# Kernel optimization log

Hardware: AMD Instinct MI355X
Metric: run time of the kernel (lower is better)

Reference implementation:

```python
import jax, jax.numpy as jnp
import numpy as np

EPS = 1e-6
N_HEADS, N_POINTS = 6, 4


def layer_norm(x, w, b):
    m = jnp.mean(x, -1, keepdims=True)
    v = jnp.mean((x - m) ** 2, -1, keepdims=True)
    return (x - m) * jax.lax.rsqrt(v + EPS) * w + b


def bilinear_sample(val, loc, Hl, Wl):
    # val: (B, nH, Hl*Wl, d); loc: (B, Lq, nH, P, 2) in [0,1]
    # matches F.grid_sample(mode='bilinear', padding='zeros', align_corners=False)
    B, nH, _, d = val.shape
    Lq, P = loc.shape[1], loc.shape[3]
    x = loc[..., 0] * Wl - 0.5
    y = loc[..., 1] * Hl - 0.5
    x0 = jnp.floor(x)
    y0 = jnp.floor(y)
    wx1 = x - x0
    wy1 = y - y0
    out = jnp.zeros((B, nH, Lq * P, d), val.dtype)
    corners = ((0, 0, (1 - wy1) * (1 - wx1)), (0, 1, (1 - wy1) * wx1),
               (1, 0, wy1 * (1 - wx1)), (1, 1, wy1 * wx1))
    for dy, dx, w in corners:
        xi = x0 + dx
        yi = y0 + dy
        valid = (xi >= 0) & (xi < Wl) & (yi >= 0) & (yi < Hl)
        xi_c = jnp.clip(xi, 0, Wl - 1).astype(jnp.int32)
        yi_c = jnp.clip(yi, 0, Hl - 1).astype(jnp.int32)
        idx = (yi_c * Wl + xi_c).transpose(0, 2, 1, 3).reshape(B, nH, Lq * P)
        g = jnp.take_along_axis(val, idx[..., None], axis=2)  # (B,nH,Lq*P,d)
        ww = jnp.where(valid, w, 0.0).transpose(0, 2, 1, 3).reshape(B, nH, Lq * P)
        out = out + g * ww[..., None]
    return out.reshape(B, nH, Lq, P, d).transpose(0, 2, 1, 3, 4)  # (B,Lq,nH,P,d)


def dwconv3x3(x, w, b):
    # x: (N, C, H, W); w: (C, 1, 3, 3) depthwise
    y = jax.lax.conv_general_dilated(x, w, (1, 1), 'SAME',
                                     feature_group_count=w.shape[0],
                                     dimension_numbers=('NCHW', 'OIHW', 'NCHW'))
    return y + b[None, :, None, None]


def setup_inputs() -> dict:
    key = jax.random.key(0)
    ks = jax.random.split(key, 16)
    B, H, W, C = 8, 32, 32, 768
    Lq = 3 * H * W
    Hf = Wf = 64
    hidden = int(C * 0.25)
    s = 0.02
    inp = {
        'query': jax.random.normal(ks[0], (B, Lq, C), jnp.float32),
        'reference_points': jax.random.uniform(ks[1], (B, Lq, 1, 2), jnp.float32),
        'feat': jax.random.normal(ks[2], (B, Hf * Wf, C), jnp.float32),
        'spatial_shapes': jnp.array([[Hf, Wf]], jnp.int32),
        'level_start_index': jnp.zeros((1,), jnp.int32),
        'H': H, 'W': W,
        'qn_w': jnp.ones((C,)), 'qn_b': jnp.zeros((C,)),
        'fn_w': jnp.ones((C,)), 'fn_b': jnp.zeros((C,)),
        'so_w': jax.random.normal(ks[3], (C, N_HEADS * N_POINTS * 2)) * s,
        'so_b': jax.random.normal(ks[4], (N_HEADS * N_POINTS * 2,)) * s,
        'aw_w': jax.random.normal(ks[5], (C, N_HEADS * N_POINTS)) * s,
        'aw_b': jnp.zeros((N_HEADS * N_POINTS,)),
        'vp_w': jax.random.normal(ks[6], (C, C)) * s,
        'vp_b': jnp.zeros((C,)),
        'op_w': jax.random.normal(ks[7], (C, C)) * s,
        'op_b': jnp.zeros((C,)),
        'ffn_w': jnp.ones((C,)), 'ffn_b': jnp.zeros((C,)),
        'fc1_w': jax.random.normal(ks[8], (C, hidden)) * s,
        'fc1_b': jnp.zeros((hidden,)),
        'dw_w': jax.random.normal(ks[9], (hidden, 1, 3, 3)) * s,
        'dw_b': jnp.zeros((hidden,)),
        'fc2_w': jax.random.normal(ks[10], (hidden, C)) * s,
        'fc2_b': jnp.zeros((C,)),
    }
    return inp


def reference(query, reference_points, feat, spatial_shapes, level_start_index, H, W,
              qn_w, qn_b, fn_w, fn_b, so_w, so_b, aw_w, aw_b, vp_w, vp_b, op_w, op_b,
              ffn_w, ffn_b, fc1_w, fc1_b, dw_w, dw_b, fc2_w, fc2_b):
    B, Lq, C = query.shape
    nH, nP = N_HEADS, N_POINTS
    d = C // nH
    ss = np.asarray(spatial_shapes)
    Hl, Wl = int(ss[0, 0]), int(ss[0, 1])

    # --- MSDeformAttn (single level) ---
    q = layer_norm(query, qn_w, qn_b)
    f = layer_norm(feat, fn_w, fn_b)
    value = (f @ vp_w + vp_b).reshape(B, Hl * Wl, nH, d).transpose(0, 2, 1, 3)  # (B,nH,Lin,d)
    offs = (q @ so_w + so_b).reshape(B, Lq, nH, 1, nP, 2)
    aw = jax.nn.softmax((q @ aw_w + aw_b).reshape(B, Lq, nH, nP), axis=-1)
    normalizer = jnp.array([Wl, Hl], query.dtype)
    loc = reference_points[:, :, None, :, None, :] + offs / normalizer  # (B,Lq,nH,1,nP,2)
    sampled = bilinear_sample(value, loc[:, :, :, 0], Hl, Wl)           # (B,Lq,nH,nP,d)
    attn = (sampled * aw[..., None]).sum(3).reshape(B, Lq, C) @ op_w + op_b
    query = query + attn

    # --- ConvFFN (3 equal HxW chunks through shared depthwise conv) ---
    x = layer_norm(query, ffn_w, ffn_b) @ fc1_w + fc1_b  # (B, 3*H*W, hid)
    n = Lq // 3
    hid = fc1_w.shape[1]
    xc = x.reshape(B, 3, n, hid).transpose(0, 1, 3, 2).reshape(B * 3, hid, H, W)
    xc = dwconv3x3(xc, dw_w, dw_b)
    x = xc.reshape(B, 3, hid, n).transpose(0, 1, 3, 2).reshape(B, Lq, hid)
    x = jax.nn.gelu(x, approximate=False)
    x = x @ fc2_w + fc2_b
    return query + x
```

## Files before the change

### kernel.cpp

```cpp
#include <hip/hip_runtime.h>
#include <hip/hip_bf16.h>
#include <math.h>

typedef __hip_bfloat16 bf16;
typedef short bf16x8 __attribute__((ext_vector_type(8)));
typedef short bf16x4 __attribute__((ext_vector_type(4)));
typedef float f32x4 __attribute__((ext_vector_type(4)));

#define NB 8
#define LQ 3072
#define CC 768
#define NHEADS 6
#define NPTS 4
#define DHEAD 128
#define HLVL 64
#define WLVL 64
#define LIN 4096
#define HID 192
#define BLTOT 24576
#define FROWS 32768

__device__ __forceinline__ float bf2f(short u)
{ return __uint_as_float(((unsigned)(unsigned short)u) << 16); }

template<int N_>
__device__ __forceinline__ void wait_vmcnt()
{
    if constexpr (N_ == 0)      asm volatile("s_waitcnt vmcnt(0)" ::: "memory");
    else if constexpr (N_ == 2) asm volatile("s_waitcnt vmcnt(2)" ::: "memory");
    else if constexpr (N_ == 4) asm volatile("s_waitcnt vmcnt(4)" ::: "memory");
    else if constexpr (N_ == 5) asm volatile("s_waitcnt vmcnt(5)" ::: "memory");
    else if constexpr (N_ == 6) asm volatile("s_waitcnt vmcnt(6)" ::: "memory");
    else if constexpr (N_ == 8) asm volatile("s_waitcnt vmcnt(8)" ::: "memory");
    else static_assert(N_ == 0, "add a vmcnt case");
}

__device__ __forceinline__ void wt_tile(float (*t)[65], const float* __restrict__ src,
                                        bf16* __restrict__ dst, int K, int N, int tn0, int tk0)
{
    const int r = threadIdx.x >> 6, c = threadIdx.x & 63;
    #pragma unroll
    for (int i = 0; i < 16; ++i)
        t[i * 4 + r][c] = src[(size_t)(tk0 + i * 4 + r) * N + tn0 + c];
    __syncthreads();
    #pragma unroll
    for (int i = 0; i < 16; ++i)
        dst[(size_t)(tn0 + i * 4 + r) * K + tk0 + c] = __float2bfloat16(t[c][i * 4 + r]);
}

__global__ __launch_bounds__(256)
void prep_kernel(const float* __restrict__ vp_w, const float* __restrict__ op_w,
                 const float* __restrict__ fc1_w, const float* __restrict__ fc2_w,
                 const float* __restrict__ so_w, const float* __restrict__ so_b,
                 const float* __restrict__ aw_w, const float* __restrict__ aw_b,
                 const float* __restrict__ feat, const float* __restrict__ fn_w,
                 const float* __restrict__ fn_b,
                 bf16* __restrict__ vp_wt, bf16* __restrict__ op_wt,
                 bf16* __restrict__ fc1_wt, bf16* __restrict__ fc2_wt,
                 bf16* __restrict__ dots_wt, float* __restrict__ db,
                 bf16* __restrict__ f_ln)
{
    __shared__ float t[64][65];
    int b = blockIdx.x;
    if (b < 144)      wt_tile(t, vp_w, vp_wt, 768, 768, (b % 12) * 64, (b / 12) * 64);
    else if (b < 288) { b -= 144; wt_tile(t, op_w, op_wt, 768, 768, (b % 12) * 64, (b / 12) * 64); }
    else if (b < 324) { b -= 288; wt_tile(t, fc1_w, fc1_wt, 768, 192, (b % 3) * 64, (b / 3) * 64); }
    else if (b < 360) { b -= 324; wt_tile(t, fc2_w, fc2_wt, 192, 768, (b % 12) * 64, (b / 12) * 64); }
    else if (b < 744) {
        b -= 360;
        int i = b * 256 + threadIdx.x;
        if (i < 128 * 768) {
            int n = i / 768, k = i - n * 768;
            float v = 0.f;
            if (n < 48) v = so_w[(size_t)k * 48 + n];
            else if (n < 72) v = aw_w[(size_t)k * 24 + (n - 48)];
            dots_wt[i] = __float2bfloat16(v);
        }
        if (i < 128) {
            float bv = 0.f;
            if (i < 48) bv = so_b[i];
            else if (i < 72) bv = aw_b[i - 48];
            db[i] = bv;
        }
    } else {
        const int row = (b - 744) * 4 + (threadIdx.x >> 6);
        const int lane = threadIdx.x & 63;
        const f32x4* xr = (const f32x4*)(feat + (size_t)row * CC);
        f32x4 f0 = xr[lane], f1 = xr[64 + lane], f2 = xr[128 + lane];
        float s = 0.f, ss = 0.f;
        #pragma unroll
        for (int k = 0; k < 4; ++k) {
            s += f0[k] + f1[k] + f2[k];
            ss += f0[k] * f0[k] + f1[k] * f1[k] + f2[k] * f2[k];
        }
        #pragma unroll
        for (int o = 32; o > 0; o >>= 1) { s += __shfl_down(s, o); ss += __shfl_down(ss, o); }
        s = __shfl(s, 0); ss = __shfl(ss, 0);
        const float m = s * (1.f / CC);
        const float rs = rsqrtf(ss * (1.f / CC) - m * m + 1e-6f);
        const f32x4* w4 = (const f32x4*)fn_w;
        const f32x4* b4 = (const f32x4*)fn_b;
        bf16* orow = f_ln + (size_t)row * CC;
        #pragma unroll
        for (int j = 0; j < 3; ++j) {
            f32x4 fj = (j == 0) ? f0 : (j == 1) ? f1 : f2;
            f32x4 wj = w4[j * 64 + lane], bj = b4[j * 64 + lane];
            bf16 t4[4];
            #pragma unroll
            for (int k = 0; k < 4; ++k) t4[k] = __float2bfloat16((fj[k] - m) * rs * wj[k] + bj[k]);
            *(bf16x4*)(orow + j * 256 + lane * 4) = *(bf16x4*)t4;
        }
    }
}

template<int BM, int BN, int WM, int WN, int MODE>
__global__ __launch_bounds__(256)
void gemm_kernel(const bf16* __restrict__ A, const bf16* __restrict__ Bt,
                 const float* __restrict__ bias, const void* __restrict__ resv,
                 void* __restrict__ outv, int M, int N, int K)
{
    constexpr int WAVES_N = BN / WN;
    constexpr int FM = WM / 16, FN = WN / 16;
    constexpr int CWA = BM / 32;
    constexpr int CWB = BN / 32;
    constexpr int LPT = CWA + CWB;
    constexpr int ABYTES = BM * 256;
    constexpr int DBUF_BYTES = (BM + BN) * 256;
    constexpr int EPI_BYTES = BM * BN * 4;
    constexpr size_t SMEM_BYTES = DBUF_BYTES > EPI_BYTES ? DBUF_BYTES : EPI_BYTES;
    __shared__ __align__(16) char smem[SMEM_BYTES];
    bf16* sA = (bf16*)smem;
    bf16* sB = (bf16*)(smem + ABYTES);
    float* epi = (float*)smem;

    const int tid = threadIdx.x;
    const int lane = tid & 63;
    const int wave = tid >> 6;

    const int nwgx = gridDim.x;
    const int nwg = nwgx * gridDim.y;
    const int bid = blockIdx.y * nwgx + blockIdx.x;
    const int swz = (bid & 7) * (nwg >> 3) + (bid >> 3);
    const int m0 = (swz / nwgx) * BM;
    const int n0 = (swz % nwgx) * BN;

    const int wm = (wave / WAVES_N) * WM;
    const int wn = (wave % WAVES_N) * WN;

    const int srow = lane >> 3;
    const int scol = ((lane & 7) ^ srow) * 8;

    constexpr int GPR8 = BN / 8;
    constexpr int GPT8 = (BM * BN / 8) / 256;
    constexpr int QPR4 = BN / 4;
    constexpr int QPT4 = (BM * BN / 4) / 256;
    float4 pr0[GPT8], pr1[GPT8];
    bf16x4 prb[QPT4];
    if constexpr (MODE == 3) {
        const float* resf = (const float*)resv;
        #pragma unroll
        for (int k = 0; k < GPT8; ++k) {
            const int f = k * 256 + tid;
            const int rr = f / GPR8, cc = (f % GPR8) * 8;
            const size_t gidx = (size_t)(m0 + rr) * N + n0 + cc;
            pr0[k] = *(const float4*)&resf[gidx];
            pr1[k] = *(const float4*)&resf[gidx + 4];
        }
    }
    if constexpr (MODE == 4) {
        const bf16* resb = (const bf16*)resv;
        #pragma unroll
        for (int k = 0; k < QPT4; ++k) {
            const int f = k * 256 + tid;
            const int rr = f / QPR4, cc = (f % QPR4) * 4;
            prb[k] = *(const bf16x4*)&resb[(size_t)(m0 + rr) * N + n0 + cc];
        }
    }

#define STAGE(tt, half)                                                                            \
    { const int k0_ = (tt) * 64;                                                                   \
      _Pragma("unroll")                                                                            \
      for (int i_ = 0; i_ < CWA; ++i_) {                                                           \
        const int c_ = i_ * 4 + wave;                                                              \
        __builtin_amdgcn_global_load_lds(                                                          \
          (const __attribute__((address_space(1))) void*)(A + (size_t)(m0 + c_ * 8 + srow) * K + k0_ + scol), \
          (__attribute__((address_space(3))) void*)(sA + (half) * (BM * 64) + c_ * 512), 16, 0, 0); } \
      _Pragma("unroll")                                                                            \
      for (int i_ = 0; i_ < CWB; ++i_) {                                                           \
        const int c_ = i_ * 4 + wave;                                                              \
        __builtin_amdgcn_global_load_lds(                                                          \
          (const __attribute__((address_space(1))) void*)(Bt + (size_t)(n0 + c_ * 8 + srow) * K + k0_ + scol), \
          (__attribute__((address_space(3))) void*)(sB + (half) * (BN * 64) + c_ * 512), 16, 0, 0); } }

    f32x4 acc[FM][FN] = {};
    const int nt = K >> 6;

    STAGE(0, 0);
    STAGE(1, 1);

    for (int t = 0; t < nt; ++t) {
        const int half = t & 1;
        if (t + 1 < nt) wait_vmcnt<LPT>();
        else            wait_vmcnt<0>();
        __builtin_amdgcn_s_barrier();
        const bf16* cA = sA + half * (BM * 64);
        const bf16* cB = sB + half * (BN * 64);
        #pragma unroll
        for (int kki = 0; kki < 2; ++kki) {
            const int kslot = kki * 4 + (lane >> 4);
            bf16x8 aF[FM], bF[FN];
            #pragma unroll
            for (int i = 0; i < FM; ++i) {
                const int row = wm + i * 16 + (lane & 15);
                aF[i] = *(const bf16x8*)(&cA[row * 64 + ((kslot ^ (row & 7)) * 8)]);
            }
            #pragma unroll
            for (int j = 0; j < FN; ++j) {
                const int row = wn + j * 16 + (lane & 15);
                bF[j] = *(const bf16x8*)(&cB[row * 64 + ((kslot ^ (row & 7)) * 8)]);
            }
            #pragma unroll
            for (int i = 0; i < FM; ++i) {
                #pragma unroll
                for (int j = 0; j < FN; ++j)
                    acc[i][j] = __builtin_amdgcn_mfma_f32_16x16x32_bf16(aF[i], bF[j], acc[i][j], 0, 0, 0);
            }
        }
        asm volatile("s_waitcnt lgkmcnt(0)" ::: "memory");
        __builtin_amdgcn_s_barrier();
        if (t + 2 < nt) STAGE(t + 2, half);
    }
#undef STAGE

    #pragma unroll
    for (int j = 0; j < FN; ++j) {
        const int colL = wn + j * 16 + (lane & 15);
        const float bj = bias[n0 + colL];
        #pragma unroll
        for (int i = 0; i < FM; ++i) {
            #pragma unroll
            for (int r = 0; r < 4; ++r) {
                const int rowL = wm + i * 16 + ((lane >> 4) << 2) + r;
                const int addr = rowL * BN + ((((colL >> 2) ^ (rowL & 7)) << 2) | (colL & 3));
                epi[addr] = acc[i][j][r] + bj;
            }
        }
    }
    __syncthreads();

    if constexpr (MODE == 0 || MODE == 3) {
        #pragma unroll
        for (int k = 0; k < GPT8; ++k) {
            const int f = k * 256 + tid;
            const int rr = f / GPR8, cc = (f % GPR8) * 8;
            const int g0 = ((cc >> 2) ^ (rr & 7)) << 2;
            const int g1 = (((cc >> 2) + 1) ^ (rr & 7)) << 2;
            float4 v0 = *(const float4*)&epi[rr * BN + g0];
            float4 v1 = *(const float4*)&epi[rr * BN + g1];
            if constexpr (MODE == 3) {
                v0.x += pr0[k].x; v0.y += pr0[k].y; v0.z += pr0[k].z; v0.w += pr0[k].w;
                v1.x += pr1[k].x; v1.y += pr1[k].y; v1.z += pr1[k].z; v1.w += pr1[k].w;
            }
            bf16 tmp[8];
            tmp[0] = __float2bfloat16(v0.x); tmp[1] = __float2bfloat16(v0.y);
            tmp[2] = __float2bfloat16(v0.z); tmp[3] = __float2bfloat16(v0.w);
            tmp[4] = __float2bfloat16(v1.x); tmp[5] = __float2bfloat16(v1.y);
            tmp[6] = __float2bfloat16(v1.z); tmp[7] = __float2bfloat16(v1.w);
            *(bf16x8*)((bf16*)outv + (size_t)(m0 + rr) * N + n0 + cc) = *(bf16x8*)tmp;
        }
    } else {
        #pragma unroll
        for (int k = 0; k < QPT4; ++k) {
            const int f = k * 256 + tid;
            const int rr = f / QPR4, cc = (f % QPR4) * 4;
            const int gs = ((cc >> 2) ^ (rr & 7)) << 2;
            float4 v = *(const float4*)&epi[rr * BN + gs];
            if constexpr (MODE == 4) {
                v.x += bf2f(prb[k][0]); v.y += bf2f(prb[k][1]);
                v.z += bf2f(prb[k][2]); v.w += bf2f(prb[k][3]);
            }
            *(float4*)&((float*)outv)[(size_t)(m0 + rr) * N + n0 + cc] = v;
        }
    }
}

__global__ __launch_bounds__(512)
void gemm_value_kernel(const bf16* __restrict__ A, const bf16* __restrict__ Bt,
                       const float* __restrict__ bias, bf16* __restrict__ outb,
                       int M, int N, int K)
{
    constexpr int BM = 128, BN = 128;
    constexpr int FM = 2, FN = 4;
    constexpr int LPT = 4;
    __shared__ __align__(16) char smem[2 * (BM + BN) * 128];
    bf16* sA = (bf16*)smem;
    bf16* sB = (bf16*)(smem + 2 * BM * 128);
    float* epi = (float*)smem;

    const int tid = threadIdx.x;
    const int lane = tid & 63;
    const int wave = tid >> 6;

    const int nwgx = gridDim.x;
    const int nwg = nwgx * gridDim.y;
    const int bid = blockIdx.y * nwgx + blockIdx.x;
    const int swz = (bid & 7) * (nwg >> 3) + (bid >> 3);
    const int m0 = (swz / nwgx) * BM;
    const int n0 = (swz % nwgx) * BN;

    const int wm = (wave >> 1) * 32;
    const int wn = (wave & 1) * 64;
    const int srow = lane >> 3;
    const int scol = ((lane & 7) ^ srow) * 8;

#define STAGEV(tt, half)                                                                           \
    { const int k0_ = (tt) * 64;                                                                   \
      _Pragma("unroll")                                                                            \
      for (int i_ = 0; i_ < 2; ++i_) {                                                             \
        const int c_ = i_ * 8 + wave;                                                              \
        __builtin_amdgcn_global_load_lds(                                                          \
          (const __attribute__((address_space(1))) void*)(A + (size_t)(m0 + c_ * 8 + srow) * K + k0_ + scol), \
          (__attribute__((address_space(3))) void*)(sA + (half) * (BM * 64) + c_ * 512), 16, 0, 0); } \
      _Pragma("unroll")                                                                            \
      for (int i_ = 0; i_ < 2; ++i_) {                                                             \
        const int c_ = i_ * 8 + wave;                                                              \
        __builtin_amdgcn_global_load_lds(                                                          \
          (const __attribute__((address_space(1))) void*)(Bt + (size_t)(n0 + c_ * 8 + srow) * K + k0_ + scol), \
          (__attribute__((address_space(3))) void*)(sB + (half) * (BN * 64) + c_ * 512), 16, 0, 0); } }

    f32x4 acc[FM][FN] = {};
    const int nt = K >> 6;

    STAGEV(0, 0);
    STAGEV(1, 1);

    for (int t = 0; t < nt; ++t) {
        const int half = t & 1;
        if (t + 1 < nt) wait_vmcnt<LPT>();
        else            wait_vmcnt<0>();
        __builtin_amdgcn_s_barrier();
        const bf16* cA = sA + half * (BM * 64);
        const bf16* cB = sB + half * (BN * 64);
        #pragma unroll
        for (int kki = 0; kki < 2; ++kki) {
            const int kslot = kki * 4 + (lane >> 4);
            bf16x8 aF[FM], bF[FN];
            #pragma unroll
            for (int i = 0; i < FM; ++i) {
                const int row = wm + i * 16 + (lane & 15);
                aF[i] = *(const bf16x8*)(&cA[row * 64 + ((kslot ^ (row & 7)) * 8)]);
            }
            #pragma unroll
            for (int j = 0; j < FN; ++j) {
                const int row = wn + j * 16 + (lane & 15);
                bF[j] = *(const bf16x8*)(&cB[row * 64 + ((kslot ^ (row & 7)) * 8)]);
            }
            #pragma unroll
            for (int i = 0; i < FM; ++i) {
                #pragma unroll
                for (int j = 0; j < FN; ++j)
                    acc[i][j] = __builtin_amdgcn_mfma_f32_16x16x32_bf16(aF[i], bF[j], acc[i][j], 0, 0, 0);
            }
        }
        asm volatile("s_waitcnt lgkmcnt(0)" ::: "memory");
        __builtin_amdgcn_s_barrier();
        if (t + 2 < nt) STAGEV(t + 2, half);
    }
#undef STAGEV

    #pragma unroll
    for (int j = 0; j < FN; ++j) {
        const int colL = wn + j * 16 + (lane & 15);
        const float bj = bias[n0 + colL];
        #pragma unroll
        for (int i = 0; i < FM; ++i) {
            #pragma unroll
            for (int r = 0; r < 4; ++r) {
                const int rowL = wm + i * 16 + ((lane >> 4) << 2) + r;
                const int addr = rowL * BN + ((((colL >> 2) ^ (rowL & 7)) << 2) | (colL & 3));
                epi[addr] = acc[i][j][r] + bj;
            }
        }
    }
    __syncthreads();
    const int hd = n0 >> 7;
    const int img = m0 >> 12;
    const int pix0 = m0 & 4095;
    bf16* obase = outb + (((size_t)img * NHEADS + hd) * LIN + pix0) * DHEAD;
    #pragma unroll
    for (int k = 0; k < 4; ++k) {
        const int f = k * 512 + tid;
        const int rr = f >> 4, cc = (f & 15) * 8;
        const int g0 = ((cc >> 2) ^ (rr & 7)) << 2;
        const int g1 = (((cc >> 2) + 1) ^ (rr & 7)) << 2;
        float4 v0 = *(const float4*)&epi[rr * BN + g0];
        float4 v1 = *(const float4*)&epi[rr * BN + g1];
        bf16 tmp[8];
        tmp[0] = __float2bfloat16(v0.x); tmp[1] = __float2bfloat16(v0.y);
        tmp[2] = __float2bfloat16(v0.z); tmp[3] = __float2bfloat16(v0.w);
        tmp[4] = __float2bfloat16(v1.x); tmp[5] = __float2bfloat16(v1.y);
        tmp[6] = __float2bfloat16(v1.z); tmp[7] = __float2bfloat16(v1.w);
        *(bf16x8*)(obase + (size_t)rr * DHEAD + cc) = *(bf16x8*)tmp;
    }
}

template<int BM, int BN, int WM, int WN, bool F32IN, int EPI>
__global__ __launch_bounds__(256)
void ln_gemm_kernel(const void* __restrict__ xv, const float* __restrict__ lnw,
                    const float* __restrict__ lnb, const bf16* __restrict__ Bt,
                    const float* __restrict__ bias, const float* __restrict__ refp,
                    void* __restrict__ outv, int M, int N)
{
    constexpr int WAVES_N = BN / WN;
    constexpr int FM = WM / 16, FN = WN / 16;
    constexpr int CWB = BN / 32;
    constexpr int RPW = BM / 4;
    static_assert(BM * BN * 4 <= 2 * BN * 64 * 2, "epi must fit in sB");
    __shared__ __align__(16) bf16 sA[BM * 768];
    __shared__ __align__(16) char sBmem[2 * BN * 64 * 2];
    bf16* sB = (bf16*)sBmem;
    float* epi = (float*)sBmem;

    const int tid = threadIdx.x;
    const int lane = tid & 63;
    const int wave = tid >> 6;

    const int nwgx = gridDim.x;
    const int nwg = nwgx * gridDim.y;
    const int bid = blockIdx.y * nwgx + blockIdx.x;
    const int swz = (bid & 7) * (nwg >> 3) + (bid >> 3);
    const int m0 = (swz / nwgx) * BM;
    const int n0 = (swz % nwgx) * BN;

    const int wm = (wave / WAVES_N) * WM;
    const int wn = (wave % WAVES_N) * WN;
    const int srow = lane >> 3;
    const int scol = ((lane & 7) ^ srow) * 8;

#define STAGEB(tt, half)                                                                           \
    { const int k0_ = (tt) * 64;                                                                   \
      _Pragma("unroll")                                                                            \
      for (int i_ = 0; i_ < CWB; ++i_) {                                                           \
        const int c_ = i_ * 4 + wave;                                                              \
        __builtin_amdgcn_global_load_lds(                                                          \
          (const __attribute__((address_space(1))) void*)(Bt + (size_t)(n0 + c_ * 8 + srow) * 768 + k0_ + scol), \
          (__attribute__((address_space(3))) void*)(sB + (half) * (BN * 64) + c_ * 512), 16, 0, 0); } }

    STAGEB(0, 0);
    STAGEB(1, 1);

    if constexpr (F32IN) {
        const f32x4* w4 = (const f32x4*)lnw;
        const f32x4* b4 = (const f32x4*)lnb;
        f32x4 wv0 = w4[lane], wv1 = w4[64 + lane], wv2 = w4[128 + lane];
        f32x4 bv0 = b4[lane], bv1 = b4[64 + lane], bv2 = b4[128 + lane];
        for (int rr = 0; rr < RPW; ++rr) {
            const int r = wave * RPW + rr;
            const f32x4* xr = (const f32x4*)((const float*)xv + (size_t)(m0 + r) * 768);
            f32x4 f0 = xr[lane], f1 = xr[64 + lane], f2 = xr[128 + lane];
            float s = 0.f, ss = 0.f;
            #pragma unroll
            for (int k = 0; k < 4; ++k) {
                s += f0[k] + f1[k] + f2[k];
                ss += f0[k] * f0[k] + f1[k] * f1[k] + f2[k] * f2[k];
            }
            #pragma unroll
            for (int o = 32; o > 0; o >>= 1) { s += __shfl_down(s, o); ss += __shfl_down(ss, o); }
            s = __shfl(s, 0); ss = __shfl(ss, 0);
            const float mn = s * (1.f / 768);
            const float rs = rsqrtf(ss * (1.f / 768) - mn * mn + 1e-6f);
            const int rx7 = r & 7;
            const int slot = (lane >> 1) & 7;
            const int off = (lane & 1) * 4;
            #pragma unroll
            for (int j = 0; j < 3; ++j) {
                f32x4 fj = (j == 0) ? f0 : (j == 1) ? f1 : f2;
                f32x4 wj = (j == 0) ? wv0 : (j == 1) ? wv1 : wv2;
                f32x4 bj = (j == 0) ? bv0 : (j == 1) ? bv1 : bv2;
                bf16 t4[4];
                #pragma unroll
                for (int k = 0; k < 4; ++k)
                    t4[k] = __float2bfloat16((fj[k] - mn) * rs * wj[k] + bj[k]);
                const int kt = j * 4 + (lane >> 4);
                *(bf16x4*)&sA[r * 768 + kt * 64 + ((slot ^ rx7) << 3) + off] = *(bf16x4*)t4;
            }
        }
    } else {
        const f32x4* w4 = (const f32x4*)lnw;
        const f32x4* b4 = (const f32x4*)lnb;
        f32x4 w80 = w4[lane * 2], w81 = w4[lane * 2 + 1], w44 = w4[128 + lane];
        f32x4 b80 = b4[lane * 2], b81 = b4[lane * 2 + 1], b44 = b4[128 + lane];
        for (int rr = 0; rr < RPW; ++rr) {
            const int r = wave * RPW + rr;
            const bf16* xr = (const bf16*)xv + (size_t)(m0 + r) * 768;
            bf16x8 v8 = *(const bf16x8*)(xr + lane * 8);
            bf16x4 v4 = *(const bf16x4*)(xr + 512 + lane * 4);
            float f[12];
            #pragma unroll
            for (int k = 0; k < 8; ++k) f[k] = bf2f(v8[k]);
            #pragma unroll
            for (int k = 0; k < 4; ++k) f[8 + k] = bf2f(v4[k]);
            float s = 0.f, ss = 0.f;
            #pragma unroll
            for (int k = 0; k < 12; ++k) { s += f[k]; ss += f[k] * f[k]; }
            #pragma unroll
            for (int o = 32; o > 0; o >>= 1) { s += __shfl_down(s, o); ss += __shfl_down(ss, o); }
            s = __shfl(s, 0); ss = __shfl(ss, 0);
            const float mn = s * (1.f / 768);
            const float rs = rsqrtf(ss * (1.f / 768) - mn * mn + 1e-6f);
            const int rx7 = r & 7;
            bf16 t8[8];
            #pragma unroll
            for (int k = 0; k < 4; ++k) t8[k] = __float2bfloat16((f[k] - mn) * rs * w80[k] + b80[k]);
            #pragma unroll
            for (int k = 0; k < 4; ++k) t8[4 + k] = __float2bfloat16((f[4 + k] - mn) * rs * w81[k] + b81[k]);
            *(bf16x8*)&sA[r * 768 + (lane >> 3) * 64 + (((lane & 7) ^ rx7) << 3)] = *(bf16x8*)t8;
            bf16 t4[4];
            #pragma unroll
            for (int k = 0; k < 4; ++k) t4[k] = __float2bfloat16((f[8 + k] - mn) * rs * w44[k] + b44[k]);
            *(bf16x4*)&sA[r * 768 + (8 + (lane >> 4)) * 64 + ((((lane >> 1) & 7) ^ rx7) << 3) + (lane & 1) * 4]
                = *(bf16x4*)t4;
        }
    }
    asm volatile("s_waitcnt lgkmcnt(0)" ::: "memory");

    f32x4 acc[FM][FN] = {};
    #pragma unroll
    for (int t = 0; t < 12; ++t) {
        const int half = t & 1;
        if (t + 1 < 12) wait_vmcnt<CWB>();
        else            wait_vmcnt<0>();
        __builtin_amdgcn_s_barrier();
        const bf16* cB = sB + half * (BN * 64);
        #pragma unroll
        for (int kki = 0; kki < 2; ++kki) {
            const int kslot = kki * 4 + (lane >> 4);
            bf16x8 aF[FM], bF[FN];
            #pragma unroll
            for (int i = 0; i < FM; ++i) {
                const int row = wm + i * 16 + (lane & 15);
                aF[i] = *(const bf16x8*)(&sA[row * 768 + t * 64 + ((kslot ^ (row & 7)) * 8)]);
            }
            #pragma unroll
            for (int j = 0; j < FN; ++j) {
                const int row = wn + j * 16 + (lane & 15);
                bF[j] = *(const bf16x8*)(&cB[row * 64 + ((kslot ^ (row & 7)) * 8)]);
            }
            #pragma unroll
            for (int i = 0; i < FM; ++i) {
                #pragma unroll
                for (int j = 0; j < FN; ++j)
                    acc[i][j] = __builtin_amdgcn_mfma_f32_16x16x32_bf16(aF[i], bF[j], acc[i][j], 0, 0, 0);
            }
        }
        asm volatile("s_waitcnt lgkmcnt(0)" ::: "memory");
        __builtin_amdgcn_s_barrier();
        if (t + 2 < 12) STAGEB(t + 2, half);
    }
#undef STAGEB

    #pragma unroll
    for (int j = 0; j < FN; ++j) {
        const int colL = wn + j * 16 + (lane & 15);
        const float bj = bias[n0 + colL];
        #pragma unroll
        for (int i = 0; i < FM; ++i) {
            #pragma unroll
            for (int r = 0; r < 4; ++r) {
                const int rowL = wm + i * 16 + ((lane >> 4) << 2) + r;
                const int addr = rowL * BN + ((((colL >> 2) ^ (rowL & 7)) << 2) | (colL & 3));
                epi[addr] = acc[i][j][r] + bj;
            }
        }
    }
    __syncthreads();

    if constexpr (EPI == 1) {
        if (tid < BM * NHEADS) {
            const int rowL = tid & (BM - 1);
            const int h = tid / BM;
            auto erd = [&](int col) -> float {
                return epi[rowL * BN + ((((col >> 2) ^ (rowL & 7)) << 2) | (col & 3))];
            };
            float l0 = erd(48 + h * 4 + 0), l1 = erd(48 + h * 4 + 1);
            float l2 = erd(48 + h * 4 + 2), l3 = erd(48 + h * 4 + 3);
            float mx = fmaxf(fmaxf(l0, l1), fmaxf(l2, l3));
            float e0 = expf(l0 - mx), e1 = expf(l1 - mx), e2 = expf(l2 - mx), e3 = expf(l3 - mx);
            float inv = 1.f / (e0 + e1 + e2 + e3);
            float ee[4] = {e0, e1, e2, e3};
            const float rx = refp[(size_t)(m0 + rowL) * 2];
            const float ry = refp[(size_t)(m0 + rowL) * 2 + 1];
            float4* pp = (float4*)outv + ((size_t)(m0 + rowL) * NHEADS + h) * 4;
            #pragma unroll
            for (int p = 0; p < 4; ++p) {
                float ox = erd(h * 8 + p * 2), oy = erd(h * 8 + p * 2 + 1);
                pp[p] = make_float4(rx + ox * (1.f / WLVL), ry + oy * (1.f / HLVL), ee[p] * inv, 0.f);
            }
        }
    } else {
        constexpr int GPR8 = BN / 8;
        constexpr int GPT8 = (BM * BN / 8) / 256;
        #pragma unroll
        for (int k = 0; k < GPT8; ++k) {
            const int f = k * 256 + tid;
            const int rr = f / GPR8, cc = (f % GPR8) * 8;
            const int g0 = ((cc >> 2) ^ (rr & 7)) << 2;
            const int g1 = (((cc >> 2) + 1) ^ (rr & 7)) << 2;
            float4 v0 = *(const float4*)&epi[rr * BN + g0];
            float4 v1 = *(const float4*)&epi[rr * BN + g1];
            bf16 tmp[8];
            tmp[0] = __float2bfloat16(v0.x); tmp[1] = __float2bfloat16(v0.y);
            tmp[2] = __float2bfloat16(v0.z); tmp[3] = __float2bfloat16(v0.w);
            tmp[4] = __float2bfloat16(v1.x); tmp[5] = __float2bfloat16(v1.y);
            tmp[6] = __float2bfloat16(v1.z); tmp[7] = __float2bfloat16(v1.w);
            *(bf16x8*)((bf16*)outv + (size_t)(m0 + rr) * N + n0 + cc) = *(bf16x8*)tmp;
        }
    }
}

__global__ __launch_bounds__(256)
void sampler_kernel(const bf16* __restrict__ value, const float4* __restrict__ params,
                    bf16* __restrict__ attn_in)
{
    const int tid = threadIdx.x;
    const int b = blockIdx.x & 7;
    const int local = blockIdx.x >> 3;
    const int h = local / 192;
    const int qc = local - h * 192;
    const int bl = b * LQ + qc * 16 + (tid >> 4);
    const int g = bl * NHEADS + h;
    const int lane16 = tid & 15;
    const bf16* vh = value + (((size_t)b * NHEADS + h) * LIN) * DHEAD + lane16 * 8;

    int offs[16];
    float wgt[16];
    #pragma unroll
    for (int p = 0; p < NPTS; ++p) {
        float4 pr = params[(size_t)g * 4 + p];
        float x = pr.x * (float)WLVL - 0.5f;
        float y = pr.y * (float)HLVL - 0.5f;
        float x0f = floorf(x), y0f = floorf(y);
        float wx1 = x - x0f, wy1 = y - y0f;
        float wx0 = 1.f - wx1, wy0 = 1.f - wy1;
        int x0 = (int)x0f, y0 = (int)y0f;
        #pragma unroll
        for (int dy = 0; dy < 2; ++dy) {
            const int yi = y0 + dy;
            const int yc = min(max(yi, 0), HLVL - 1);
            const float wy = (dy ? wy1 : wy0) * ((yi >= 0 && yi < HLVL) ? pr.z : 0.f);
            #pragma unroll
            for (int dx = 0; dx < 2; ++dx) {
                const int xi = x0 + dx;
                const int xc = min(max(xi, 0), WLVL - 1);
                const int idx = p * 4 + dy * 2 + dx;
                offs[idx] = (yc * WLVL + xc) * DHEAD;
                wgt[idx] = wy * (dx ? wx1 : wx0) * ((xi >= 0 && xi < WLVL) ? 1.f : 0.f);
            }
        }
    }
    bf16x8 v[16];
    #pragma unroll
    for (int i = 0; i < 16; ++i) v[i] = *(const bf16x8*)(vh + offs[i]);
    float acc[8] = {};
    #pragma unroll
    for (int i = 0; i < 16; ++i) {
        #pragma unroll
        for (int j = 0; j < 8; ++j)
            acc[j] += wgt[i] * bf2f(v[i][j]);
    }
    bf16 tmp[8];
    #pragma unroll
    for (int j = 0; j < 8; ++j) tmp[j] = __float2bfloat16(acc[j]);
    *(bf16x8*)(attn_in + (size_t)bl * CC + h * DHEAD + lane16 * 8) = *(bf16x8*)tmp;
}

__global__ __launch_bounds__(192)
void dwconv_gelu_kernel(const bf16* __restrict__ z, const float* __restrict__ dw_w,
                        const float* __restrict__ dw_b, bf16* __restrict__ g)
{
    const int tp = threadIdx.x / 48;
    const int tc = threadIdx.x % 48;
    const int m = blockIdx.x * 4 + tp;
    const int c = tc * 4;
    const int pix = m & 1023;
    const int h = pix >> 5, w = pix & 31;
    float acc[4];
    #pragma unroll
    for (int j = 0; j < 4; ++j) acc[j] = dw_b[c + j];
    #pragma unroll
    for (int dy = -1; dy <= 1; ++dy) {
        int hh2 = h + dy;
        if (hh2 < 0 || hh2 >= 32) continue;
        #pragma unroll
        for (int dx = -1; dx <= 1; ++dx) {
            int ww2 = w + dx;
            if (ww2 < 0 || ww2 >= 32) continue;
            bf16x4 vv = *(const bf16x4*)&z[(size_t)(m + dy * 32 + dx) * HID + c];
            #pragma unroll
            for (int j = 0; j < 4; ++j)
                acc[j] += bf2f(vv[j]) * dw_w[(c + j) * 9 + (dy + 1) * 3 + (dx + 1)];
        }
    }
    bf16 tmp[4];
    #pragma unroll
    for (int j = 0; j < 4; ++j) {
        float ge = acc[j] * 0.5f * (1.f + erff(acc[j] * 0.70710678118f));
        tmp[j] = __float2bfloat16(ge);
    }
    *(bf16x4*)&g[(size_t)m * HID + c] = *(bf16x4*)tmp;
}

extern "C" void kernel_launch(void* const* d_in, const int* in_sizes, int n_in,
                              void* d_out, int out_size, void* d_ws, size_t ws_size,
                              hipStream_t stream)
{
    const float* query = (const float*)d_in[0];
    const float* refp  = (const float*)d_in[1];
    const float* feat  = (const float*)d_in[2];
    const float* qn_w = (const float*)d_in[7];
    const float* qn_b = (const float*)d_in[8];
    const float* fn_w = (const float*)d_in[9];
    const float* fn_b = (const float*)d_in[10];
    const float* so_w = (const float*)d_in[11];
    const float* so_b = (const float*)d_in[12];
    const float* aw_w = (const float*)d_in[13];
    const float* aw_b = (const float*)d_in[14];
    const float* vp_w = (const float*)d_in[15];
    const float* vp_b = (const float*)d_in[16];
    const float* op_w = (const float*)d_in[17];
    const float* op_b = (const float*)d_in[18];
    const float* ffn_w = (const float*)d_in[19];
    const float* ffn_b = (const float*)d_in[20];
    const float* fc1_w = (const float*)d_in[21];
    const float* fc1_b = (const float*)d_in[22];
    const float* dw_w = (const float*)d_in[23];
    const float* dw_b = (const float*)d_in[24];
    const float* fc2_w = (const float*)d_in[25];
    const float* fc2_b = (const float*)d_in[26];
    float* out = (float*)d_out;

    if (ws_size < (size_t)125829632) return;
    char* ws = (char*)d_ws;
    bf16* vp_wt   = (bf16*)(ws + 0);
    bf16* op_wt   = (bf16*)(ws + 1179648);
    bf16* fc1_wt  = (bf16*)(ws + 2359296);
    bf16* fc2_wt  = (bf16*)(ws + 2654208);
    bf16* dots_wt = (bf16*)(ws + 2949120);
    float* dots_b = (float*)(ws + 3145728);
    char* paramsR = ws + 3146240;
    char* dotsR   = ws + 12583424;
    char* regA = ws + 25166336;
    char* regB = ws + 75497984;
    float4* params = (float4*)paramsR;
    bf16* g        = (bf16*)paramsR;
    bf16* z        = (bf16*)dotsR;
    bf16* f_ln    = (bf16*)regA;
    bf16* attn_in = (bf16*)regA;
    bf16* value = (bf16*)regB;
    bf16* s_bf  = (bf16*)regB;

    prep_kernel<<<744 + FROWS / 4, 256, 0, stream>>>(
        vp_w, op_w, fc1_w, fc2_w, so_w, so_b, aw_w, aw_b, feat, fn_w, fn_b,
        vp_wt, op_wt, fc1_wt, fc2_wt, dots_wt, dots_b, f_ln);

    ln_gemm_kernel<32, 128, 16, 64, true, 1><<<dim3(1, BLTOT / 32), 256, 0, stream>>>(
        query, qn_w, qn_b, dots_wt, dots_b, refp, params, BLTOT, 128);
    gemm_value_kernel<<<dim3(6, FROWS / 128), 512, 0, stream>>>(
        f_ln, vp_wt, vp_b, value, FROWS, 768, 768);
    sampler_kernel<<<(BLTOT * NHEADS) / 16, 256, 0, stream>>>(value, params, attn_in);
    gemm_kernel<64, 128, 32, 64, 3><<<dim3(6, BLTOT / 64), 256, 0, stream>>>(
        attn_in, op_wt, op_b, query, s_bf, BLTOT, 768, 768);

    ln_gemm_kernel<32, 64, 32, 16, false, 0><<<dim3(3, BLTOT / 32), 256, 0, stream>>>(
        s_bf, ffn_w, ffn_b, fc1_wt, fc1_b, nullptr, z, BLTOT, HID);
    dwconv_gelu_kernel<<<BLTOT / 4, 192, 0, stream>>>(z, dw_w, dw_b, g);
    gemm_kernel<64, 128, 32, 64, 4><<<dim3(6, BLTOT / 64), 256, 0, stream>>>(
        g, fc2_wt, fc2_b, s_bf, out, BLTOT, 768, HID);
}
```

Baseline: 303.4 us.

## Fuse value projection GEMM and query LN+offset GEMM into one launch

After: 292.1 us (median of 6 runs). 1.04x faster.

```diff
diff --git a/kernel.cpp b/kernel.cpp
--- a/kernel.cpp
+++ b/kernel.cpp
@@ -29,7 +29,6 @@
     if constexpr (N_ == 0)      asm volatile("s_waitcnt vmcnt(0)" ::: "memory");
     else if constexpr (N_ == 2) asm volatile("s_waitcnt vmcnt(2)" ::: "memory");
     else if constexpr (N_ == 4) asm volatile("s_waitcnt vmcnt(4)" ::: "memory");
-    else if constexpr (N_ == 5) asm volatile("s_waitcnt vmcnt(5)" ::: "memory");
     else if constexpr (N_ == 6) asm volatile("s_waitcnt vmcnt(6)" ::: "memory");
     else if constexpr (N_ == 8) asm volatile("s_waitcnt vmcnt(8)" ::: "memory");
     else static_assert(N_ == 0, "add a vmcnt case");
@@ -284,15 +283,17 @@
     }
 }
 
-__global__ __launch_bounds__(512)
-void gemm_value_kernel(const bf16* __restrict__ A, const bf16* __restrict__ Bt,
-                       const float* __restrict__ bias, bf16* __restrict__ outb,
-                       int M, int N, int K)
+#define VAL_BLOCKS 1536
+#define DOTS_BLOCKS 768
+
+__device__ void value_body(char* smem,
+                           const bf16* __restrict__ A, const bf16* __restrict__ Bt,
+                           const float* __restrict__ bias, bf16* __restrict__ outb)
 {
     constexpr int BM = 128, BN = 128;
     constexpr int FM = 2, FN = 4;
     constexpr int LPT = 4;
-    __shared__ __align__(16) char smem[2 * (BM + BN) * 128];
+    constexpr int K = 768;
     bf16* sA = (bf16*)smem;
     bf16* sB = (bf16*)(smem + 2 * BM * 128);
     float* epi = (float*)smem;
@@ -301,12 +302,10 @@
     const int lane = tid & 63;
     const int wave = tid >> 6;
 
-    const int nwgx = gridDim.x;
-    const int nwg = nwgx * gridDim.y;
-    const int bid = blockIdx.y * nwgx + blockIdx.x;
-    const int swz = (bid & 7) * (nwg >> 3) + (bid >> 3);
-    const int m0 = (swz / nwgx) * BM;
-    const int n0 = (swz % nwgx) * BN;
+    const int bid = blockIdx.x;
+    const int swz = (bid & 7) * (VAL_BLOCKS >> 3) + (bid >> 3);
+    const int m0 = (swz / 6) * BM;
+    const int n0 = (swz % 6) * BN;
 
     const int wm = (wave >> 1) * 32;
     const int wn = (wave & 1) * 64;
@@ -329,14 +328,12 @@
           (__attribute__((address_space(3))) void*)(sB + (half) * (BN * 64) + c_ * 512), 16, 0, 0); } }
 
     f32x4 acc[FM][FN] = {};
-    const int nt = K >> 6;
-
     STAGEV(0, 0);
     STAGEV(1, 1);
 
-    for (int t = 0; t < nt; ++t) {
+    for (int t = 0; t < 12; ++t) {
         const int half = t & 1;
-        if (t + 1 < nt) wait_vmcnt<LPT>();
+        if (t + 1 < 12) wait_vmcnt<LPT>();
         else            wait_vmcnt<0>();
         __builtin_amdgcn_s_barrier();
         const bf16* cA = sA + half * (BM * 64);
@@ -364,7 +361,7 @@
         }
         asm volatile("s_waitcnt lgkmcnt(0)" ::: "memory");
         __builtin_amdgcn_s_barrier();
-        if (t + 2 < nt) STAGEV(t + 2, half);
+        if (t + 2 < 12) STAGEV(t + 2, half);
     }
 #undef STAGEV
 
@@ -404,59 +401,52 @@
     }
 }
 
-template<int BM, int BN, int WM, int WN, bool F32IN, int EPI>
-__global__ __launch_bounds__(256)
-void ln_gemm_kernel(const void* __restrict__ xv, const float* __restrict__ lnw,
-                    const float* __restrict__ lnb, const bf16* __restrict__ Bt,
-                    const float* __restrict__ bias, const float* __restrict__ refp,
-                    void* __restrict__ outv, int M, int N)
-{
-    constexpr int WAVES_N = BN / WN;
-    constexpr int FM = WM / 16, FN = WN / 16;
-    constexpr int CWB = BN / 32;
-    constexpr int RPW = BM / 4;
-    static_assert(BM * BN * 4 <= 2 * BN * 64 * 2, "epi must fit in sB");
-    __shared__ __align__(16) bf16 sA[BM * 768];
-    __shared__ __align__(16) char sBmem[2 * BN * 64 * 2];
-    bf16* sB = (bf16*)sBmem;
-    float* epi = (float*)sBmem;
+__device__ void dots_body(char* smem,
+                          const float* __restrict__ query, const float* __restrict__ lnw,
+                          const float* __restrict__ lnb, const bf16* __restrict__ Bt,
+                          const float* __restrict__ bias, const float* __restrict__ refp,
+                          float4* __restrict__ params)
+{
+    constexpr int BM = 32, BN = 128;
+    constexpr int FM = 1, FN = 2;
+    bf16* sA = (bf16*)smem;
+    bf16* sB = (bf16*)(smem + BM * 768 * 2);
+    float* epi = (float*)sB;
 
     const int tid = threadIdx.x;
     const int lane = tid & 63;
     const int wave = tid >> 6;
 
-    const int nwgx = gridDim.x;
-    const int nwg = nwgx * gridDim.y;
-    const int bid = blockIdx.y * nwgx + blockIdx.x;
-    const int swz = (bid & 7) * (nwg >> 3) + (bid >> 3);
-    const int m0 = (swz / nwgx) * BM;
-    const int n0 = (swz % nwgx) * BN;
-
-    const int wm = (wave / WAVES_N) * WM;
-    const int wn = (wave % WAVES_N) * WN;
+    const int bid = blockIdx.x - VAL_BLOCKS;
+    const int swz = (bid & 7) * (DOTS_BLOCKS >> 3) + (bid >> 3);
+    const int m0 = swz * BM;
+
+    const int wm = (wave >> 2) * 16;
+    const int wn = (wave & 3) * 32;
     const int srow = lane >> 3;
     const int scol = ((lane & 7) ^ srow) * 8;
 
-#define STAGEB(tt, half)                                                                           \
+#define STAGED(tt, half)                                                                           \
     { const int k0_ = (tt) * 64;                                                                   \
       _Pragma("unroll")                                                                            \
-      for (int i_ = 0; i_ < CWB; ++i_) {                                                           \
-        const int c_ = i_ * 4 + wave;                                                              \
+      for (int i_ = 0; i_ < 2; ++i_) {                                                             \
+        const int c_ = i_ * 8 + wave;                                                              \
         __builtin_amdgcn_global_load_lds(                                                          \
-          (const __attribute__((address_space(1))) void*)(Bt + (size_t)(n0 + c_ * 8 + srow) * 768 + k0_ + scol), \
+          (const __attribute__((address_space(1))) void*)(Bt + (size_t)(c_ * 8 + srow) * 768 + k0_ + scol), \
           (__attribute__((address_space(3))) void*)(sB + (half) * (BN * 64) + c_ * 512), 16, 0, 0); } }
 
-    STAGEB(0, 0);
-    STAGEB(1, 1);
-
-    if constexpr (F32IN) {
+    STAGED(0, 0);
+    STAGED(1, 1);
+
+    {
         const f32x4* w4 = (const f32x4*)lnw;
         const f32x4* b4 = (const f32x4*)lnb;
         f32x4 wv0 = w4[lane], wv1 = w4[64 + lane], wv2 = w4[128 + lane];
         f32x4 bv0 = b4[lane], bv1 = b4[64 + lane], bv2 = b4[128 + lane];
-        for (int rr = 0; rr < RPW; ++rr) {
-            const int r = wave * RPW + rr;
-            const f32x4* xr = (const f32x4*)((const float*)xv + (size_t)(m0 + r) * 768);
+        #pragma unroll
+        for (int rr = 0; rr < 4; ++rr) {
+            const int r = wave * 4 + rr;
+            const f32x4* xr = (const f32x4*)(query + (size_t)(m0 + r) * 768);
             f32x4 f0 = xr[lane], f1 = xr[64 + lane], f2 = xr[128 + lane];
             float s = 0.f, ss = 0.f;
             #pragma unroll
@@ -485,14 +475,147 @@
                 *(bf16x4*)&sA[r * 768 + kt * 64 + ((slot ^ rx7) << 3) + off] = *(bf16x4*)t4;
             }
         }
-    } else {
+    }
+    asm volatile("s_waitcnt lgkmcnt(0)" ::: "memory");
+
+    f32x4 acc[FM][FN] = {};
+    #pragma unroll
+    for (int t = 0; t < 12; ++t) {
+        const int half = t & 1;
+        if (t + 1 < 12) wait_vmcnt<2>();
+        else            wait_vmcnt<0>();
+        __builtin_amdgcn_s_barrier();
+        const bf16* cB = sB + half * (BN * 64);
+        #pragma unroll
+        for (int kki = 0; kki < 2; ++kki) {
+            const int kslot = kki * 4 + (lane >> 4);
+            bf16x8 aF[FM], bF[FN];
+            #pragma unroll
+            for (int i = 0; i < FM; ++i) {
+                const int row = wm + i * 16 + (lane & 15);
+                aF[i] = *(const bf16x8*)(&sA[row * 768 + t * 64 + ((kslot ^ (row & 7)) * 8)]);
+            }
+            #pragma unroll
+            for (int j = 0; j < FN; ++j) {
+                const int row = wn + j * 16 + (lane & 15);
+                bF[j] = *(const bf16x8*)(&cB[row * 64 + ((kslot ^ (row & 7)) * 8)]);
+            }
+            #pragma unroll
+            for (int i = 0; i < FM; ++i) {
+                #pragma unroll
+                for (int j = 0; j < FN; ++j)
+                    acc[i][j] = __builtin_amdgcn_mfma_f32_16x16x32_bf16(aF[i], bF[j], acc[i][j], 0, 0, 0);
+            }
+        }
+        asm volatile("s_waitcnt lgkmcnt(0)" ::: "memory");
+        __builtin_amdgcn_s_barrier();
+        if (t + 2 < 12) STAGED(t + 2, half);
+    }
+#undef STAGED
+
+    #pragma unroll
+    for (int j = 0; j < FN; ++j) {
+        const int colL = wn + j * 16 + (lane & 15);
+        const float bj = bias[colL];
+        #pragma unroll
+        for (int r = 0; r < 4; ++r) {
+            const int rowL = wm + ((lane >> 4) << 2) + r;
+            const int addr = rowL * BN + ((((colL >> 2) ^ (rowL & 7)) << 2) | (colL & 3));
+            epi[addr] = acc[0][j][r] + bj;
+        }
+    }
+    __syncthreads();
+
+    if (tid < BM * NHEADS) {
+        const int rowL = tid & (BM - 1);
+        const int h = tid / BM;
+        auto erd = [&](int col) -> float {
+            return epi[rowL * BN + ((((col >> 2) ^ (rowL & 7)) << 2) | (col & 3))];
+        };
+        float l0 = erd(48 + h * 4 + 0), l1 = erd(48 + h * 4 + 1);
+        float l2 = erd(48 + h * 4 + 2), l3 = erd(48 + h * 4 + 3);
+        float mx = fmaxf(fmaxf(l0, l1), fmaxf(l2, l3));
+        float e0 = expf(l0 - mx), e1 = expf(l1 - mx), e2 = expf(l2 - mx), e3 = expf(l3 - mx);
+        float inv = 1.f / (e0 + e1 + e2 + e3);
+        float ee[4] = {e0, e1, e2, e3};
+        const float rx = refp[(size_t)(m0 + rowL) * 2];
+        const float ry = refp[(size_t)(m0 + rowL) * 2 + 1];
+        float4* pp = params + ((size_t)(m0 + rowL) * NHEADS + h) * 4;
+        #pragma unroll
+        for (int p = 0; p < 4; ++p) {
+            float ox = erd(h * 8 + p * 2), oy = erd(h * 8 + p * 2 + 1);
+            pp[p] = make_float4(rx + ox * (1.f / WLVL), ry + oy * (1.f / HLVL), ee[p] * inv, 0.f);
+        }
+    }
+}
+
+__global__ __launch_bounds__(512)
+void fused_value_dots_kernel(const bf16* __restrict__ f_ln, const bf16* __restrict__ vp_wt,
+                             const float* __restrict__ vp_b, bf16* __restrict__ value,
+                             const float* __restrict__ query, const float* __restrict__ qn_w,
+                             const float* __restrict__ qn_b, const bf16* __restrict__ dots_wt,
+                             const float* __restrict__ dots_b, const float* __restrict__ refp,
+                             float4* __restrict__ params)
+{
+    __shared__ __align__(16) char smem[81920];
+    if (blockIdx.x < VAL_BLOCKS)
+        value_body(smem, f_ln, vp_wt, vp_b, value);
+    else
+        dots_body(smem, query, qn_w, qn_b, dots_wt, dots_b, refp, params);
+}
+
+template<int BM, int BN, int WM, int WN>
+__global__ __launch_bounds__(256)
+void ln_gemm_kernel(const bf16* __restrict__ xv, const float* __restrict__ lnw,
+                    const float* __restrict__ lnb, const bf16* __restrict__ Bt,
+                    const float* __restrict__ bias, bf16* __restrict__ outv, int M, int N)
+{
+    constexpr int WAVES_N = BN / WN;
+    constexpr int FM = WM / 16, FN = WN / 16;
+    constexpr int CWB = BN / 32;
+    constexpr int RPW = BM / 4;
+    static_assert(BM * BN * 4 <= 2 * BN * 64 * 2, "epi must fit in sB");
+    __shared__ __align__(16) bf16 sA[BM * 768];
+    __shared__ __align__(16) char sBmem[2 * BN * 64 * 2];
+    bf16* sB = (bf16*)sBmem;
+    float* epi = (float*)sBmem;
+
+    const int tid = threadIdx.x;
+    const int lane = tid & 63;
+    const int wave = tid >> 6;
+
+    const int nwgx = gridDim.x;
+    const int nwg = nwgx * gridDim.y;
+    const int bid = blockIdx.y * nwgx + blockIdx.x;
+    const int swz = (bid & 7) * (nwg >> 3) + (bid >> 3);
+    const int m0 = (swz / nwgx) * BM;
+    const int n0 = (swz % nwgx) * BN;
+
+    const int wm = (wave / WAVES_N) * WM;
+    const int wn = (wave % WAVES_N) * WN;
+    const int srow = lane >> 3;
+    const int scol = ((lane & 7) ^ srow) * 8;
+
+#define STAGEB(tt, half)                                                                           \
+    { const int k0_ = (tt) * 64;                                                                   \
+      _Pragma("unroll")                                                                            \
+      for (int i_ = 0; i_ < CWB; ++i_) {                                                           \
+        const int c_ = i_ * 4 + wave;                                                              \
+        __builtin_amdgcn_global_load_lds(                                                          \
+          (const __attribute__((address_space(1))) void*)(Bt + (size_t)(n0 + c_ * 8 + srow) * 768 + k0_ + scol), \
+          (__attribute__((address_space(3))) void*)(sB + (half) * (BN * 64) + c_ * 512), 16, 0, 0); } }
+
+    STAGEB(0, 0);
+    STAGEB(1, 1);
+
+    {
         const f32x4* w4 = (const f32x4*)lnw;
         const f32x4* b4 = (const f32x4*)lnb;
         f32x4 w80 = w4[lane * 2], w81 = w4[lane * 2 + 1], w44 = w4[128 + lane];
         f32x4 b80 = b4[lane * 2], b81 = b4[lane * 2 + 1], b44 = b4[128 + lane];
         for (int rr = 0; rr < RPW; ++rr) {
             const int r = wave * RPW + rr;
-            const bf16* xr = (const bf16*)xv + (size_t)(m0 + r) * 768;
+            const bf16* xr = xv + (size_t)(m0 + r) * 768;
             bf16x8 v8 = *(const bf16x8*)(xr + lane * 8);
             bf16x4 v4 = *(const bf16x4*)(xr + 512 + lane * 4);
             float f[12];
@@ -575,46 +698,22 @@
     }
     __syncthreads();
 
-    if constexpr (EPI == 1) {
-        if (tid < BM * NHEADS) {
-            const int rowL = tid & (BM - 1);
-            const int h = tid / BM;
-            auto erd = [&](int col) -> float {
-                return epi[rowL * BN + ((((col >> 2) ^ (rowL & 7)) << 2) | (col & 3))];
-            };
-            float l0 = erd(48 + h * 4 + 0), l1 = erd(48 + h * 4 + 1);
-            float l2 = erd(48 + h * 4 + 2), l3 = erd(48 + h * 4 + 3);
-            float mx = fmaxf(fmaxf(l0, l1), fmaxf(l2, l3));
-            float e0 = expf(l0 - mx), e1 = expf(l1 - mx), e2 = expf(l2 - mx), e3 = expf(l3 - mx);
-            float inv = 1.f / (e0 + e1 + e2 + e3);
-            float ee[4] = {e0, e1, e2, e3};
-            const float rx = refp[(size_t)(m0 + rowL) * 2];
-            const float ry = refp[(size_t)(m0 + rowL) * 2 + 1];
-            float4* pp = (float4*)outv + ((size_t)(m0 + rowL) * NHEADS + h) * 4;
-            #pragma unroll
-            for (int p = 0; p < 4; ++p) {
-                float ox = erd(h * 8 + p * 2), oy = erd(h * 8 + p * 2 + 1);
-                pp[p] = make_float4(rx + ox * (1.f / WLVL), ry + oy * (1.f / HLVL), ee[p] * inv, 0.f);
-            }
-        }
-    } else {
-        constexpr int GPR8 = BN / 8;
-        constexpr int GPT8 = (BM * BN / 8) / 256;
-        #pragma unroll
-        for (int k = 0; k < GPT8; ++k) {
-            const int f = k * 256 + tid;
-            const int rr = f / GPR8, cc = (f % GPR8) * 8;
-            const int g0 = ((cc >> 2) ^ (rr & 7)) << 2;
-            const int g1 = (((cc >> 2) + 1) ^ (rr & 7)) << 2;
-            float4 v0 = *(const float4*)&epi[rr * BN + g0];
-            float4 v1 = *(const float4*)&epi[rr * BN + g1];
-            bf16 tmp[8];
-            tmp[0] = __float2bfloat16(v0.x); tmp[1] = __float2bfloat16(v0.y);
-            tmp[2] = __float2bfloat16(v0.z); tmp[3] = __float2bfloat16(v0.w);
-            tmp[4] = __float2bfloat16(v1.x); tmp[5] = __float2bfloat16(v1.y);
-            tmp[6] = __float2bfloat16(v1.z); tmp[7] = __float2bfloat16(v1.w);
-            *(bf16x8*)((bf16*)outv + (size_t)(m0 + rr) * N + n0 + cc) = *(bf16x8*)tmp;
-        }
+    constexpr int GPR8 = BN / 8;
+    constexpr int GPT8 = (BM * BN / 8) / 256;
+    #pragma unroll
+    for (int k = 0; k < GPT8; ++k) {
+        const int f = k * 256 + tid;
+        const int rr = f / GPR8, cc = (f % GPR8) * 8;
+        const int g0 = ((cc >> 2) ^ (rr & 7)) << 2;
+        const int g1 = (((cc >> 2) + 1) ^ (rr & 7)) << 2;
+        float4 v0 = *(const float4*)&epi[rr * BN + g0];
+        float4 v1 = *(const float4*)&epi[rr * BN + g1];
+        bf16 tmp[8];
+        tmp[0] = __float2bfloat16(v0.x); tmp[1] = __float2bfloat16(v0.y);
+        tmp[2] = __float2bfloat16(v0.z); tmp[3] = __float2bfloat16(v0.w);
+        tmp[4] = __float2bfloat16(v1.x); tmp[5] = __float2bfloat16(v1.y);
+        tmp[6] = __float2bfloat16(v1.z); tmp[7] = __float2bfloat16(v1.w);
+        *(bf16x8*)(outv + (size_t)(m0 + rr) * N + n0 + cc) = *(bf16x8*)tmp;
     }
 }
 
@@ -763,16 +862,14 @@
         vp_w, op_w, fc1_w, fc2_w, so_w, so_b, aw_w, aw_b, feat, fn_w, fn_b,
         vp_wt, op_wt, fc1_wt, fc2_wt, dots_wt, dots_b, f_ln);
 
-    ln_gemm_kernel<32, 128, 16, 64, true, 1><<<dim3(1, BLTOT / 32), 256, 0, stream>>>(
-        query, qn_w, qn_b, dots_wt, dots_b, refp, params, BLTOT, 128);
-    gemm_value_kernel<<<dim3(6, FROWS / 128), 512, 0, stream>>>(
-        f_ln, vp_wt, vp_b, value, FROWS, 768, 768);
+    fused_value_dots_kernel<<<VAL_BLOCKS + DOTS_BLOCKS, 512, 0, stream>>>(
+        f_ln, vp_wt, vp_b, value, query, qn_w, qn_b, dots_wt, dots_b, refp, params);
     sampler_kernel<<<(BLTOT * NHEADS) / 16, 256, 0, stream>>>(value, params, attn_in);
     gemm_kernel<64, 128, 32, 64, 3><<<dim3(6, BLTOT / 64), 256, 0, stream>>>(
         attn_in, op_wt, op_b, query, s_bf, BLTOT, 768, 768);
 
-    ln_gemm_kernel<32, 64, 32, 16, false, 0><<<dim3(3, BLTOT / 32), 256, 0, stream>>>(
-        s_bf, ffn_w, ffn_b, fc1_wt, fc1_b, nullptr, z, BLTOT, HID);
+    ln_gemm_kernel<32, 64, 32, 16><<<dim3(3, BLTOT / 32), 256, 0, stream>>>(
+        s_bf, ffn_w, ffn_b, fc1_wt, fc1_b, z, BLTOT, HID);
     dwconv_gelu_kernel<<<BLTOT / 4, 192, 0, stream>>>(z, dw_w, dw_b, g);
     gemm_kernel<64, 128, 32, 64, 4><<<dim3(6, BLTOT / 64), 256, 0, stream>>>(
         g, fc2_wt, fc2_b, s_bf, out, BLTOT, 768, HID);
```
